# Optimization experiments

Measured on AMD Instinct MI355X. Metric: run time of the kernel, lower is better.

The kernel has to match this reference:

```python
import jax, jax.numpy as jnp
import numpy as np

D_MODEL = 2048
N_HEADS = 8
N_KV = 4
HEAD_DIM = 256
WINDOW = 1024
EPS = 1e-6
ROPE_BASE = 10000.0


def _rms_norm(x, w):
    # x: [..., D]; matches torch: x * rsqrt(mean(x^2) + eps) * w
    return x * jax.lax.rsqrt(jnp.mean(x * x, axis=-1, keepdims=True) + EPS) * w


def _rope_cos_sin(pos):
    # pos: [T] ints -> cos/sin: [T, HEAD_DIM] (cat(freqs, freqs) as in source)
    inv_freq = 1.0 / (ROPE_BASE ** (jnp.arange(0, HEAD_DIM, 2, dtype=jnp.float32) / HEAD_DIM))
    freqs = pos.astype(jnp.float32)[:, None] * inv_freq[None, :]  # [T, D/2]
    emb = jnp.concatenate([freqs, freqs], axis=-1)                # [T, D]
    return jnp.cos(emb), jnp.sin(emb)


def _apply_rotary(x, cos, sin):
    # x: [B, H, T, D]; interleaved rotate-half exactly as the torch code
    x1 = x[..., 0::2]
    x2 = x[..., 1::2]
    x_rot = jnp.stack([-x2, x1], axis=-1).reshape(x.shape)
    return x * cos[None, None, :, :] + x_rot * sin[None, None, :, :]


def setup_inputs() -> dict:
    key = jax.random.key(0)
    ks = jax.random.split(key, 8)
    B, T = 1, 4096
    s = 0.02
    return {
        "x": jax.random.normal(ks[0], (B, T, D_MODEL), dtype=jnp.float32),
        "pos": jnp.arange(T, dtype=jnp.int32),
        "Wq": jax.random.normal(ks[1], (N_HEADS * HEAD_DIM, D_MODEL), dtype=jnp.float32) * s,
        "Wk": jax.random.normal(ks[2], (N_KV * HEAD_DIM, D_MODEL), dtype=jnp.float32) * s,
        "Wv": jax.random.normal(ks[3], (N_KV * HEAD_DIM, D_MODEL), dtype=jnp.float32) * s,
        "Wo": jax.random.normal(ks[4], (D_MODEL, N_HEADS * HEAD_DIM), dtype=jnp.float32) * s,
        "q_norm_w": jnp.ones((HEAD_DIM,), dtype=jnp.float32),
        "k_norm_w": jnp.ones((HEAD_DIM,), dtype=jnp.float32),
    }


def reference(x, pos, Wq, Wk, Wv, Wo, q_norm_w, k_norm_w):
    B, T, _ = x.shape
    # projections (torch Linear: y = x @ W.T)
    q = (x @ Wq.T).reshape(B, T, N_HEADS, HEAD_DIM).transpose(0, 2, 1, 3)  # [B,H,T,D]
    k = (x @ Wk.T).reshape(B, T, N_KV, HEAD_DIM).transpose(0, 2, 1, 3)    # [B,Hkv,T,D]
    v = (x @ Wv.T).reshape(B, T, N_KV, HEAD_DIM).transpose(0, 2, 1, 3)
    # per-head RMSNorm
    q = _rms_norm(q, q_norm_w)
    k = _rms_norm(k, k_norm_w)
    # RoPE
    cos, sin = _rope_cos_sin(pos)
    q = _apply_rotary(q, cos, sin)
    k = _apply_rotary(k, cos, sin)
    # GQA repeat: [B,Hkv,T,D] -> [B,H,T,D]
    rep = N_HEADS // N_KV
    k = jnp.repeat(k, rep, axis=1)
    v = jnp.repeat(v, rep, axis=1)
    # full scores + sliding-window causal mask (faithful to source)
    scores = jnp.einsum("bhqd,bhkd->bhqk", q, k) / jnp.sqrt(jnp.float32(HEAD_DIM))
    i = jnp.arange(T)[:, None]
    j = jnp.arange(T)[None, :]
    allowed = (j <= i) & (j >= i - WINDOW + 1)  # [T,T]
    scores = jnp.where(allowed[None, None, :, :], scores, -jnp.inf)
    attn = jax.nn.softmax(scores, axis=-1)
    y = jnp.einsum("bhqk,bhkd->bhqd", attn, v)
    y = y.transpose(0, 2, 1, 3).reshape(B, T, N_HEADS * HEAD_DIM)
    return y @ Wo.T
```

## Files before the change

### kernel.cpp

```cpp
#include <hip/hip_runtime.h>
#include <cstdint>
#include <cmath>

typedef __bf16 bf16x8 __attribute__((ext_vector_type(8)));
typedef float  f32x4  __attribute__((ext_vector_type(4)));

#define DEVI __device__ __forceinline__

#define SEQ 4096
#define NH 8
#define NKV 4
#define HD 256
#define WIN 1024

DEVI void gload16(const void* g, void* l) {
  __builtin_amdgcn_global_load_lds((const __attribute__((address_space(1))) void*)g,
                                   (__attribute__((address_space(3))) void*)l,
                                   16, 0, 0);
}

DEVI bf16x8 ld8f(const float* p) {
  const f32x4 a = *(const f32x4*)p;
  const f32x4 b = *(const f32x4*)(p + 4);
  bf16x8 r;
#pragma unroll
  for (int j = 0; j < 4; ++j) { r[j] = (__bf16)a[j]; r[4 + j] = (__bf16)b[j]; }
  return r;
}

DEVI void st1(float* p, float v)  { *p = v; }
DEVI void st1(__bf16* p, float v) { *p = (__bf16)v; }

DEVI void barx() {
  asm volatile("" ::: "memory");
  __builtin_amdgcn_s_barrier();
  asm volatile("" ::: "memory");
}

__global__ __launch_bounds__(256)
void cvt_all(const float* __restrict__ x,  const float* __restrict__ wq,
             const float* __restrict__ wk, const float* __restrict__ wv,
             const float* __restrict__ wo,
             __bf16* __restrict__ xb, __bf16* __restrict__ wqkvb,
             __bf16* __restrict__ wob) {
  const size_t g = (size_t)blockIdx.x * 256 + threadIdx.x;
  const float* src; __bf16* dst; size_t off;
  if      (g < 1048576) { src = x;  dst = xb;               off = g; }
  else if (g < 1572864) { src = wq; dst = wqkvb;            off = g - 1048576; }
  else if (g < 1835008) { src = wk; dst = wqkvb + 4194304;  off = g - 1572864; }
  else if (g < 2097152) { src = wv; dst = wqkvb + 6291456;  off = g - 1835008; }
  else                  { src = wo; dst = wob;              off = g - 2097152; }
  *(bf16x8*)(dst + off * 8) = ld8f(src + off * 8);
}

template <int BM, typename TC>
__global__ __launch_bounds__(512, 2)
void gemm256(const __bf16* __restrict__ A, const __bf16* __restrict__ B,
             TC* __restrict__ C, int N, int K) {
  constexpr int AI    = BM / 128;
  constexpr int MF    = BM / 32;
  constexpr int AUNIT = BM * 64;
  constexpr int ASZ   = 4 * AUNIT;
  constexpr int VMC   = 2 * (AI + 2);
  __shared__ char lds[ASZ + 65536];

  const int tid  = threadIdx.x;
  const int lane = tid & 63;
  const int wave = tid >> 6;
  const int l15  = lane & 15;
  const int l4   = lane >> 4;
  const int wm   = wave >> 2;
  const int wn   = wave & 3;

  constexpr int nTm = 4096 / BM;
  const int lin  = blockIdx.x;
  const int xcd  = lin & 7;
  const int kk   = lin >> 3;
  const int nTn  = N >> 8;
  const int rowT = kk % nTm;
  const int colT = xcd * (nTn >> 3) + kk / nTm;
  const int row0 = rowT * BM;
  const int col0 = colT << 8;

  const int srow = tid >> 2;
  const int scol = ((tid & 3) ^ ((tid >> 3) & 3)) << 3;
  const __bf16* Asrc = A + (size_t)(row0 + srow) * K + scol;
  const __bf16* Bsrc = B + (size_t)(col0 + srow) * K + scol;

  const int swz  = (l4 ^ ((l15 >> 1) & 3)) << 4;
  const int aoff = (wm * (BM / 2) + l15) * 64 + swz;
  const int boff = ((wn << 6) + l15) * 64 + swz;

  auto stA = [&](int kx, int h, int b) {
    int k0 = kx << 6; if (k0 >= K) k0 = 0;
    const __bf16* s = Asrc + k0 + (h << 5);
    char* d = lds + (b * 2 + h) * AUNIT + wave * 1024;
#pragma unroll
    for (int i = 0; i < AI; ++i)
      gload16(s + (size_t)(i << 7) * K, d + i * 8192);
  };
  auto stB = [&](int kx, int h, int b) {
    int k0 = kx << 6; if (k0 >= K) k0 = 0;
    const __bf16* s = Bsrc + k0 + (h << 5);
    char* d = lds + ASZ + (b * 2 + h) * 16384 + wave * 1024;
#pragma unroll
    for (int i = 0; i < 2; ++i)
      gload16(s + (size_t)(i << 7) * K, d + i * 8192);
  };

  f32x4 acc[MF][4] = {};

  stA(0, 0, 0); stB(0, 0, 0);
  stA(0, 1, 0); stB(0, 1, 0);
  stA(1, 0, 1); stB(1, 0, 1);

  const int NT = K >> 6;
  for (int kt = 0; kt < NT; ++kt) {
    const int b = kt & 1, nb = b ^ 1;
#pragma unroll
    for (int half = 0; half < 2; ++half) {
      asm volatile("s_waitcnt vmcnt(%0)" :: "i"(VMC) : "memory");
      barx();
      bf16x8 af[4], ag[4], bfr[4];
      const char* pa = lds + (b * 2 + half) * AUNIT + aoff;
      const char* pb = lds + ASZ + (b * 2 + half) * 16384 + boff;
#pragma unroll
      for (int m = 0; m < 4; ++m) af[m] = *(const bf16x8*)(pa + (m << 10));
#pragma unroll
      for (int n = 0; n < 4; ++n) bfr[n] = *(const bf16x8*)(pb + (n << 10));
      if constexpr (BM == 256) {
#pragma unroll
        for (int m = 0; m < 4; ++m) ag[m] = *(const bf16x8*)(pa + 4096 + (m << 10));
      }
      if (half == 0) { stA(kt + 1, 1, nb); stB(kt + 1, 1, nb); }
      else           { stA(kt + 2, 0, b);  stB(kt + 2, 0, b);  }
      __builtin_amdgcn_s_setprio(1);
#pragma unroll
      for (int m = 0; m < 4; ++m)
#pragma unroll
        for (int n = 0; n < 4; ++n)
          acc[m][n] = __builtin_amdgcn_mfma_f32_16x16x32_bf16(af[m], bfr[n], acc[m][n], 0, 0, 0);
      if constexpr (BM == 256) {
#pragma unroll
        for (int m = 0; m < 4; ++m)
#pragma unroll
          for (int n = 0; n < 4; ++n)
            acc[4 + m][n] = __builtin_amdgcn_mfma_f32_16x16x32_bf16(ag[m], bfr[n], acc[4 + m][n], 0, 0, 0);
      }
      __builtin_amdgcn_s_setprio(0);
    }
  }

#pragma unroll
  for (int mf = 0; mf < MF; ++mf) {
    const int rb = row0 + wm * (BM / 2) + (mf >> 2) * 64 + (mf & 3) * 16 + (l4 << 2);
#pragma unroll
    for (int reg = 0; reg < 4; ++reg) {
      TC* crow = C + (size_t)(rb + reg) * N + col0 + (wn << 6) + l15;
#pragma unroll
      for (int n = 0; n < 4; ++n) st1(crow + (n << 4), acc[mf][n][reg]);
    }
  }
}

__global__ __launch_bounds__(256)
void norm_rope_tv(__bf16* __restrict__ qkv, __bf16* __restrict__ Vt,
                  const float* __restrict__ qw, const float* __restrict__ kw,
                  const int* __restrict__ pos) {
  if (blockIdx.x < 12288) {
    const int gw   = blockIdx.x * 4 + (threadIdx.x >> 6);
    const int lane = threadIdx.x & 63;
    __bf16* base; const float* w; int t;
    if (gw < SEQ * NH) {
      t = gw >> 3;
      base = qkv + (size_t)t * 4096 + (gw & 7) * HD;
      w = qw;
    } else {
      const int g = gw - SEQ * NH;
      t = g >> 2;
      base = qkv + (size_t)t * 4096 + 2048 + (g & 3) * HD;
      w = kw;
    }

    const int d0 = lane * 4;
    float v[4]; float ss = 0.f;
#pragma unroll
    for (int j = 0; j < 4; ++j) { v[j] = (float)base[d0 + j]; ss += v[j] * v[j]; }
#pragma unroll
    for (int off = 1; off < 64; off <<= 1) ss += __shfl_xor(ss, off);
    const float rms = rsqrtf(ss * (1.0f / 256.0f) + 1e-6f);
    const float p = (float)pos[t];

    float n[4];
#pragma unroll
    for (int j = 0; j < 4; ++j) n[j] = v[j] * rms * w[d0 + j];

    float outv[4];
#pragma unroll
    for (int e = 0; e < 4; e += 2) {
      const int i0 = d0 + e, i1 = i0 + 1;
      const float f0 = exp2f(-(float)(i0 & 127) * 0.103810253f);
      const float f1 = exp2f(-(float)(i1 & 127) * 0.103810253f);
      float s0, cc0, s1, cc1;
      sincosf(p * f0, &s0, &cc0);
      sincosf(p * f1, &s1, &cc1);
      outv[e]     = n[e] * cc0 - n[e + 1] * s0;
      outv[e + 1] = n[e + 1] * cc1 + n[e] * s1;
    }
#pragma unroll
    for (int j = 0; j < 4; ++j) base[d0 + j] = (__bf16)outv[j];
  } else {
    __shared__ __bf16 tile[64][72];
    const int b   = blockIdx.x - 12288;
    const int tid = threadIdx.x;
    const int tb  = (b & 63) * 64;
    const int yy  = b >> 6;
    const int kvh = yy >> 2;
    const int db  = (yy & 3) * 64;
#pragma unroll
    for (int i = 0; i < 2; ++i) {
      const int s = i * 256 + tid;
      const int r = s >> 3, c = (s & 7) * 8;
      bf16x8 val = *(const bf16x8*)(qkv + (size_t)(tb + r) * 4096 + 3072 + kvh * HD + db + c);
#pragma unroll
      for (int j = 0; j < 8; ++j) tile[r][c + j] = val[j];
    }
    __syncthreads();
#pragma unroll
    for (int i = 0; i < 2; ++i) {
      const int s = i * 256 + tid;
      const int r = s >> 3, c = (s & 7) * 8;
      bf16x8 outv;
#pragma unroll
      for (int j = 0; j < 8; ++j) outv[j] = tile[c + j][r];
      *(bf16x8*)(Vt + (size_t)(kvh * HD + db + r) * SEQ + tb + c) = outv;
    }
  }
}

__global__ __launch_bounds__(256, 2)
void attn_fwd(const __bf16* __restrict__ qkv, const __bf16* __restrict__ Vt,
              __bf16* __restrict__ Y) {
  __shared__ __bf16 Ks2[8][64][32];
  __shared__ __bf16 Vts2[2][256][32];
  __shared__ __bf16 Ps[4][16][72];
  const int tid  = threadIdx.x;
  const int lane = tid & 63;
  const int wave = tid >> 6;
  const int l15  = lane & 15;
  const int l4   = lane >> 4;
  const int q0   = blockIdx.x * 64;
  const int head = blockIdx.y;
  const int kvh  = head >> 1;
  const int qw   = q0 + wave * 16;

  bf16x8 qf[8];
  const __bf16* qrow = qkv + (size_t)(qw + l15) * 4096 + head * HD;
#pragma unroll
  for (int ks = 0; ks < 8; ++ks) {
    bf16x8 t = *(const bf16x8*)(qrow + ks * 32 + l4 * 8);
#pragma unroll
    for (int j = 0; j < 8; ++j) t[j] = (__bf16)((float)t[j] * 0.0625f);
    qf[ks] = t;
  }

  f32x4 o[16] = {};
  float l_run[4] = {0.f, 0.f, 0.f, 0.f};

  int lo = q0 - (WIN - 1); if (lo < 0) lo = 0;
  const int kt0 = lo >> 6;
  const int kt1 = (q0 + 63) >> 6;

  for (int kt = kt0; kt <= kt1; ++kt) {
    const int kb = kt * 64;
    __syncthreads();
#pragma unroll
    for (int i = 0; i < 8; ++i) {
      const int s = i * 256 + tid;
      gload16(qkv + (size_t)(kb + ((s >> 2) & 63)) * 4096 + 2048 + kvh * HD
                  + (s >> 8) * 32 + (s & 3) * 8,
              (char*)Ks2 + (i * 256 + wave * 64) * 16);
    }
#pragma unroll
    for (int i = 0; i < 8; ++i) {
      const int s = i * 256 + tid;
      gload16(Vt + ((size_t)kvh * HD + ((s >> 2) & 255)) * SEQ + kb
                 + (s >> 10) * 32 + (s & 3) * 8,
              (char*)Vts2 + (i * 256 + wave * 64) * 16);
    }
    __syncthreads();

    f32x4 s_acc[4] = {};
#pragma unroll
    for (int kn = 0; kn < 4; ++kn) {
#pragma unroll
      for (int ks = 0; ks < 8; ++ks) {
        bf16x8 kf = *(const bf16x8*)&Ks2[ks][kn * 16 + l15][l4 * 8];
        s_acc[kn] = __builtin_amdgcn_mfma_f32_16x16x32_bf16(qf[ks], kf, s_acc[kn], 0, 0, 0);
      }
    }

#pragma unroll
    for (int reg = 0; reg < 4; ++reg) {
      const int r  = l4 * 4 + reg;
      const int qg = qw + r;
      float ps = 0.f;
#pragma unroll
      for (int kn = 0; kn < 4; ++kn) {
        const int kg = kb + kn * 16 + l15;
        const bool ok = (kg <= qg) && (kg > qg - WIN);
        const float p = ok ? __expf(fminf(s_acc[kn][reg], 34.f) - 34.f) : 0.f;
        ps += p;
        Ps[wave][r][kn * 16 + l15] = (__bf16)p;
      }
      l_run[reg] += ps;
    }

#pragma unroll
    for (int ks2 = 0; ks2 < 2; ++ks2) {
      bf16x8 pf = *(const bf16x8*)&Ps[wave][l15][ks2 * 32 + l4 * 8];
#pragma unroll
      for (int dn = 0; dn < 16; ++dn) {
        bf16x8 vf = *(const bf16x8*)&Vts2[ks2][dn * 16 + l15][l4 * 8];
        o[dn] = __builtin_amdgcn_mfma_f32_16x16x32_bf16(pf, vf, o[dn], 0, 0, 0);
      }
    }
  }

#pragma unroll
  for (int reg = 0; reg < 4; ++reg) {
#pragma unroll
    for (int off = 1; off < 16; off <<= 1)
      l_run[reg] += __shfl_xor(l_run[reg], off);
    const float inv = 1.0f / l_run[reg];
    const int q = qw + l4 * 4 + reg;
    __bf16* yrow = Y + ((size_t)q * NH + head) * HD + l15;
#pragma unroll
    for (int dn = 0; dn < 16; ++dn)
      yrow[dn * 16] = (__bf16)(o[dn][reg] * inv);
  }
}

extern "C" void kernel_launch(void* const* d_in, const int* in_sizes, int n_in,
                              void* d_out, int out_size, void* d_ws, size_t ws_size,
                              hipStream_t stream) {
  (void)in_sizes; (void)n_in; (void)out_size; (void)ws_size;
  const float* x   = (const float*)d_in[0];
  const int*   pos = (const int*)d_in[1];
  const float* Wq  = (const float*)d_in[2];
  const float* Wk  = (const float*)d_in[3];
  const float* Wv  = (const float*)d_in[4];
  const float* Wo  = (const float*)d_in[5];
  const float* qw  = (const float*)d_in[6];
  const float* kw  = (const float*)d_in[7];
  float* out = (float*)d_out;

  char* ws = (char*)d_ws;
  const size_t MB = 1024 * 1024;
  __bf16* qkv_ws = (__bf16*)(ws);
  __bf16* vt_ws  = (__bf16*)(ws + 32 * MB);
  __bf16* y_ws   = (__bf16*)(ws + 40 * MB);
  __bf16* xb     = (__bf16*)(ws + 56 * MB);
  __bf16* wqkvb  = (__bf16*)(ws + 72 * MB);
  __bf16* wob    = (__bf16*)(ws + 88 * MB);

  cvt_all<<<dim3(10240), dim3(256), 0, stream>>>(x, Wq, Wk, Wv, Wo, xb, wqkvb, wob);
  gemm256<256, __bf16><<<dim3(256), dim3(512), 0, stream>>>(xb, wqkvb, qkv_ws, 4096, 2048);
  norm_rope_tv<<<dim3(13312), dim3(256), 0, stream>>>(qkv_ws, vt_ws, qw, kw, pos);
  attn_fwd<<<dim3(64, 8), dim3(256), 0, stream>>>(qkv_ws, vt_ws, y_ws);
  gemm256<128, float><<<dim3(256), dim3(512), 0, stream>>>(y_ws, wob, out, 2048, 2048);
}
```

Before: 318.3 us.

## Double-buffer K/V tiles in attention with async prefetch and swizzled LDS

The attention kernel now loads 32-key K and V tiles into two LDS buffers, prefetching tile kt+2 while tile kt is computed, and waits with a partial vmcnt instead of a full sync. This is meant to hide global load latency behind MFMA work. The LDS layout is XOR-swizzled to cut bank conflicts. The change also raises wave priority around MFMA sections and flattens the grid so that heads interleave across blocks. Smaller tiles mean more barriers per key, and the prefetch past the end is clamped to the last tile.

After: 317.2 us. Within noise of the previous version (-0.3%).

```diff
diff --git a/kernel.cpp b/kernel.cpp
--- a/kernel.cpp
+++ b/kernel.cpp
@@ -241,16 +241,17 @@
 __global__ __launch_bounds__(256, 2)
 void attn_fwd(const __bf16* __restrict__ qkv, const __bf16* __restrict__ Vt,
               __bf16* __restrict__ Y) {
-  __shared__ __bf16 Ks2[8][64][32];
-  __shared__ __bf16 Vts2[2][256][32];
-  __shared__ __bf16 Ps[4][16][72];
+  __shared__ char klds[2][16384];
+  __shared__ char vlds[2][16384];
+  __shared__ __bf16 Ps[4][16][40];
   const int tid  = threadIdx.x;
   const int lane = tid & 63;
   const int wave = tid >> 6;
   const int l15  = lane & 15;
   const int l4   = lane >> 4;
-  const int q0   = blockIdx.x * 64;
-  const int head = blockIdx.y;
+  const int lin  = blockIdx.x;
+  const int head = lin & 7;
+  const int q0   = (lin >> 3) * 64;
   const int kvh  = head >> 1;
   const int qw   = q0 + wave * 16;
 
@@ -268,37 +269,56 @@
   float l_run[4] = {0.f, 0.f, 0.f, 0.f};
 
   int lo = q0 - (WIN - 1); if (lo < 0) lo = 0;
-  const int kt0 = lo >> 6;
-  const int kt1 = (q0 + 63) >> 6;
+  const int kt0 = lo >> 5;
+  const int kt1 = (q0 + 63) >> 5;
+  const int kbmax = kt1 << 5;
+
+  const int skey = (tid >> 2) & 31;
+  const int sdim = tid >> 2;
+  const int sg   = (tid & 3) ^ ((tid >> 3) & 3);
+  const int sth  = tid >> 7;
+
+  auto stK = [&](int kt, int b) {
+    int kb = kt << 5; if (kb > kbmax) kb = kbmax;
+    const __bf16* s = qkv + (size_t)(kb + skey) * 4096 + 2048 + kvh * HD
+                          + sth * 32 + sg * 8;
+    char* d = klds[b] + wave * 1024;
+#pragma unroll
+    for (int i = 0; i < 4; ++i)
+      gload16(s + i * 64, d + i * 4096);
+  };
+  auto stV = [&](int kt, int b) {
+    int kb = kt << 5; if (kb > kbmax) kb = kbmax;
+    const __bf16* s = Vt + ((size_t)kvh * HD + sdim) * SEQ + kb + sg * 8;
+    char* d = vlds[b] + wave * 1024;
+#pragma unroll
+    for (int i = 0; i < 4; ++i)
+      gload16(s + (size_t)i * 64 * SEQ, d + i * 4096);
+  };
+
+  stK(kt0, 0);     stV(kt0, 0);
+  stK(kt0 + 1, 1); stV(kt0 + 1, 1);
+
+  const int rswz = (l4 ^ ((l15 >> 1) & 3)) << 4;
 
   for (int kt = kt0; kt <= kt1; ++kt) {
-    const int kb = kt * 64;
-    __syncthreads();
-#pragma unroll
-    for (int i = 0; i < 8; ++i) {
-      const int s = i * 256 + tid;
-      gload16(qkv + (size_t)(kb + ((s >> 2) & 63)) * 4096 + 2048 + kvh * HD
-                  + (s >> 8) * 32 + (s & 3) * 8,
-              (char*)Ks2 + (i * 256 + wave * 64) * 16);
-    }
-#pragma unroll
-    for (int i = 0; i < 8; ++i) {
-      const int s = i * 256 + tid;
-      gload16(Vt + ((size_t)kvh * HD + ((s >> 2) & 255)) * SEQ + kb
-                 + (s >> 10) * 32 + (s & 3) * 8,
-              (char*)Vts2 + (i * 256 + wave * 64) * 16);
-    }
-    __syncthreads();
-
-    f32x4 s_acc[4] = {};
-#pragma unroll
-    for (int kn = 0; kn < 4; ++kn) {
+    const int p  = (kt - kt0) & 1;
+    const int kb = kt << 5;
+    asm volatile("s_waitcnt vmcnt(8)" ::: "memory");
+    barx();
+
+    const char* kbase = klds[p];
+    f32x4 s_acc[2] = {};
+    __builtin_amdgcn_s_setprio(1);
+#pragma unroll
+    for (int kn = 0; kn < 2; ++kn) {
 #pragma unroll
       for (int ks = 0; ks < 8; ++ks) {
-        bf16x8 kf = *(const bf16x8*)&Ks2[ks][kn * 16 + l15][l4 * 8];
+        bf16x8 kf = *(const bf16x8*)(kbase + (ks * 32 + kn * 16 + l15) * 64 + rswz);
         s_acc[kn] = __builtin_amdgcn_mfma_f32_16x16x32_bf16(qf[ks], kf, s_acc[kn], 0, 0, 0);
       }
     }
+    __builtin_amdgcn_s_setprio(0);
 
 #pragma unroll
     for (int reg = 0; reg < 4; ++reg) {
@@ -306,26 +326,31 @@
       const int qg = qw + r;
       float ps = 0.f;
 #pragma unroll
-      for (int kn = 0; kn < 4; ++kn) {
+      for (int kn = 0; kn < 2; ++kn) {
         const int kg = kb + kn * 16 + l15;
         const bool ok = (kg <= qg) && (kg > qg - WIN);
-        const float p = ok ? __expf(fminf(s_acc[kn][reg], 34.f) - 34.f) : 0.f;
-        ps += p;
-        Ps[wave][r][kn * 16 + l15] = (__bf16)p;
+        const float pv = ok ? __expf(fminf(s_acc[kn][reg], 34.f) - 34.f) : 0.f;
+        ps += pv;
+        Ps[wave][r][kn * 16 + l15] = (__bf16)pv;
       }
       l_run[reg] += ps;
     }
 
-#pragma unroll
-    for (int ks2 = 0; ks2 < 2; ++ks2) {
-      bf16x8 pf = *(const bf16x8*)&Ps[wave][l15][ks2 * 32 + l4 * 8];
-#pragma unroll
-      for (int dn = 0; dn < 16; ++dn) {
-        bf16x8 vf = *(const bf16x8*)&Vts2[ks2][dn * 16 + l15][l4 * 8];
-        o[dn] = __builtin_amdgcn_mfma_f32_16x16x32_bf16(pf, vf, o[dn], 0, 0, 0);
-      }
-    }
-  }
+    const char* vbase = vlds[p];
+    bf16x8 pf = *(const bf16x8*)&Ps[wave][l15][l4 * 8];
+    __builtin_amdgcn_s_setprio(1);
+#pragma unroll
+    for (int dn = 0; dn < 16; ++dn) {
+      bf16x8 vf = *(const bf16x8*)(vbase + (dn * 16 + l15) * 64 + rswz);
+      o[dn] = __builtin_amdgcn_mfma_f32_16x16x32_bf16(pf, vf, o[dn], 0, 0, 0);
+    }
+    __builtin_amdgcn_s_setprio(0);
+
+    barx();
+    stK(kt + 2, p);
+    stV(kt + 2, p);
+  }
+  asm volatile("s_waitcnt vmcnt(0)" ::: "memory");
 
 #pragma unroll
   for (int reg = 0; reg < 4; ++reg) {
@@ -367,6 +392,6 @@
   cvt_all<<<dim3(10240), dim3(256), 0, stream>>>(x, Wq, Wk, Wv, Wo, xb, wqkvb, wob);
   gemm256<256, __bf16><<<dim3(256), dim3(512), 0, stream>>>(xb, wqkvb, qkv_ws, 4096, 2048);
   norm_rope_tv<<<dim3(13312), dim3(256), 0, stream>>>(qkv_ws, vt_ws, qw, kw, pos);
-  attn_fwd<<<dim3(64, 8), dim3(256), 0, stream>>>(qkv_ws, vt_ws, y_ws);
+  attn_fwd<<<dim3(512), dim3(256), 0, stream>>>(qkv_ws, vt_ws, y_ws);
   gemm256<128, float><<<dim3(256), dim3(512), 0, stream>>>(y_ws, wob, out, 2048, 2048);
 }
```
